# Performance work log

Measured on AMD Instinct MI355X. Metric: run time of the kernel, lower is better.

The kernel has to match this reference:

```python
import jax, jax.numpy as jnp
import numpy as np

S, B, D, H, DH = 2048, 2, 512, 8, 64
SCALE = 1.0 / DH ** 0.5
EPS = 1e-5
LN_EPS = 1e-5


def setup_inputs() -> dict:
    key = jax.random.key(0)
    k1, k2, k3, k4 = jax.random.split(key, 4)
    h = jax.random.normal(k1, (S, B, D), dtype=jnp.float32)
    # causal mask, True = masked out, shape [qlen, klen, 1] (dim==3 branch)
    attn_mask = jnp.triu(jnp.ones((S, S), dtype=bool), k=1)[:, :, None]
    Wq = jax.random.normal(k2, (D, H * DH), dtype=jnp.float32) * 0.02
    Wkv = jax.random.normal(k3, (D, 2 * H * DH), dtype=jnp.float32) * 0.02
    Wo = jax.random.normal(k4, (H * DH, D), dtype=jnp.float32) * 0.02
    gamma = jnp.ones((D,), dtype=jnp.float32)
    beta = jnp.zeros((D,), dtype=jnp.float32)
    return {"h": h, "Wq": Wq, "Wkv": Wkv, "Wo": Wo,
            "gamma": gamma, "beta": beta, "attn_mask": attn_mask}


def _layer_norm(x, gamma, beta):
    mu = jnp.mean(x, axis=-1, keepdims=True)
    var = jnp.mean(jnp.square(x - mu), axis=-1, keepdims=True)
    return (x - mu) * jax.lax.rsqrt(var + LN_EPS) * gamma + beta


def reference(h, Wq, Wkv, Wo, gamma, beta, attn_mask):
    # mems=None, pre_lnorm=False, dropout=dropatt=0 (eval)
    c = h
    head_q = (h @ Wq).reshape(S, B, H, DH)
    kv = (c @ Wkv)
    head_k, head_v = jnp.split(kv, 2, axis=-1)
    head_k = head_k.reshape(S, B, H, DH)
    head_v = head_v.reshape(S, B, H, DH)
    # elu(x) + 1 feature map
    head_q = jax.nn.elu(head_q) + 1.0
    head_k = jax.nn.elu(head_k) + 1.0
    # quadratic score matrix [i, j, b, n]
    attn_score = jnp.einsum('ibnd,jbnd->ijbn', head_q, head_k) * SCALE
    # dim==3 mask: [qlen, klen, 1] -> [qlen, klen, 1, 1], fill with 0
    attn_score = jnp.where(attn_mask[:, :, :, None], 0.0, attn_score)
    # sum-normalize over key axis (dim 1 = j)
    denominator = jnp.sum(attn_score, axis=1, keepdims=True) + EPS
    attn_prob = attn_score / denominator
    attn_vec = jnp.einsum('ijbn,jbnd->ibnd', attn_prob, head_v)
    attn_vec = attn_vec.reshape(S, B, H * DH)
    attn_out = attn_vec @ Wo
    # post-lnorm residual
    return _layer_norm(h + attn_out, gamma, beta)
```

## Files before the change

### kernel.cpp

```cpp
#include <hip/hip_runtime.h>
#include <hip/hip_bf16.h>
#include <math.h>

#define SCALE 0.125f
#define EPS 1e-5f
#define LN_EPS 1e-5f

typedef short short8 __attribute__((ext_vector_type(8)));
typedef float floatx4 __attribute__((ext_vector_type(4)));
typedef unsigned short us;

__device__ __forceinline__ float elu1(float x) { return x > 0.f ? x + 1.f : __expf(x); }
__device__ __forceinline__ us f2bf(float f) {
    __hip_bfloat16 b = __float2bfloat16(f);
    return __builtin_bit_cast(us, b);
}
__device__ __forceinline__ void gload_lds16(const void* g, void* lds) {
    __builtin_amdgcn_global_load_lds(
        (const __attribute__((address_space(1))) unsigned int*)g,
        (__attribute__((address_space(3))) unsigned int*)lds, 16, 0, 0);
}
__device__ __forceinline__ floatx4 mfma_bf16(short8 a, short8 b, floatx4 c) {
    return __builtin_amdgcn_mfma_f32_16x16x32_bf16(a, b, c, 0, 0, 0);
}

__global__ __launch_bounds__(256)
void pack_kernel(const float* __restrict__ h, const float* __restrict__ Wq,
                 const float* __restrict__ Wkv, const float* __restrict__ Wo,
                 us* __restrict__ hB, us* __restrict__ WqkvT, us* __restrict__ WoT,
                 us* __restrict__ VTg) {
    const int bid = blockIdx.x, tid = threadIdx.x;
    if (bid < 2048) {
        int idx = bid * 1024 + tid * 4;
        float4 v = *(const float4*)(h + idx);
        ushort4 o;
        o.x = f2bf(v.x); o.y = f2bf(v.y); o.z = f2bf(v.z); o.w = f2bf(v.w);
        *(ushort4*)(hB + idx) = o;
        return;
    }
    if (bid < 2304) {
        __shared__ us T[64][72];
        const float* src; int ld, n0s, k0; us* dst;
        if (bid < 2240) {
            int t2 = bid - 2048;
            int nt = t2 % 24, kt = t2 / 24;
            int n0 = nt * 64; k0 = kt * 64;
            if (n0 < 512) { src = Wq; ld = 512; n0s = n0; }
            else          { src = Wkv; ld = 1024; n0s = n0 - 512; }
            dst = WqkvT + (size_t)n0 * 512;
        } else {
            int t2 = bid - 2240;
            int nt = t2 & 7, kt = t2 >> 3;
            src = Wo; ld = 512; n0s = nt * 64; k0 = kt * 64;
            dst = WoT + (size_t)(nt * 64) * 512;
        }
        {
            int k = tid >> 2, cs = (tid & 3) * 16;
            const float* p = src + (size_t)(k0 + k) * ld + n0s + cs;
#pragma unroll
            for (int q = 0; q < 4; ++q) {
                float4 v = *(const float4*)(p + q * 4);
                T[k][cs + q * 4 + 0] = f2bf(v.x);
                T[k][cs + q * 4 + 1] = f2bf(v.y);
                T[k][cs + q * 4 + 2] = f2bf(v.z);
                T[k][cs + q * 4 + 3] = f2bf(v.w);
            }
        }
        __syncthreads();
        {
            int n = tid >> 2, ks = (tid & 3) * 16;
            __align__(16) us tmp[16];
#pragma unroll
            for (int j = 0; j < 16; ++j) tmp[j] = T[ks + j][n];
            us* po = dst + (size_t)n * 512 + k0 + ks;
            *(uint4*)(po) = *(uint4*)(tmp);
            *(uint4*)(po + 8) = *(uint4*)(tmp + 8);
        }
        return;
    }
    {
        int e = (bid - 2304) * 1024 + tid * 4;
        int chain = e >> 11, s = e & 2047;
        ushort4 o; o.x = 0x3f80; o.y = 0x3f80; o.z = 0x3f80; o.w = 0x3f80;
        *(ushort4*)(VTg + ((size_t)(chain * 80 + 64)) * 2048 + s) = o;
    }
}

__global__ __launch_bounds__(256)
void qkv_gemm(const us* __restrict__ A, const us* __restrict__ BT,
              us* __restrict__ Qg, us* __restrict__ Kg, us* __restrict__ Vg) {
    __shared__ __align__(16) us As[2][128 * 32];
    __shared__ __align__(16) us Bs[2][128 * 32];
    const int tid = threadIdx.x;
    const int w = tid >> 6, l = tid & 63;
    const int m0 = blockIdx.y * 128, n0 = blockIdx.x * 128;
    const int wm = (w >> 1) * 64, wn = (w & 1) * 64;
    floatx4 acc[4][4];
#pragma unroll
    for (int i = 0; i < 4; ++i)
#pragma unroll
        for (int j = 0; j < 4; ++j)
#pragma unroll
            for (int e = 0; e < 4; ++e) acc[i][j][e] = 0.f;

    auto STAGE = [&](int buf, int kt) {
#pragma unroll
        for (int r = 0; r < 2; ++r) {
            int slot = (r * 4 + w) * 64 + l;
            int row = slot >> 2, part = slot & 3;
            int g = part ^ (row & 3);
            gload_lds16(A + (size_t)(m0 + row) * 512 + kt + g * 8, &As[buf][(r * 4 + w) * 512]);
            gload_lds16(BT + (size_t)(n0 + row) * 512 + kt + g * 8, &Bs[buf][(r * 4 + w) * 512]);
        }
    };

    STAGE(0, 0);
    __syncthreads();
    for (int t = 0; t < 16; ++t) {
        int cur = t & 1;
        if (t < 15) STAGE(cur ^ 1, (t + 1) * 32);
        short8 a[4], b[4];
#pragma unroll
        for (int mi = 0; mi < 4; ++mi) {
            int row = wm + mi * 16 + (l & 15);
            int p = (l >> 4) ^ (row & 3);
            a[mi] = *(const short8*)(&As[cur][row * 32 + p * 8]);
        }
#pragma unroll
        for (int ni = 0; ni < 4; ++ni) {
            int row = wn + ni * 16 + (l & 15);
            int p = (l >> 4) ^ (row & 3);
            b[ni] = *(const short8*)(&Bs[cur][row * 32 + p * 8]);
        }
#pragma unroll
        for (int mi = 0; mi < 4; ++mi)
#pragma unroll
            for (int ni = 0; ni < 4; ++ni)
                acc[mi][ni] = mfma_bf16(a[mi], b[ni], acc[mi][ni]);
        __syncthreads();
    }
    const int region = blockIdx.x >> 2;
    us* outp = region == 0 ? Qg : (region == 1 ? Kg : Vg);
    const int cb = n0 - region * 512;
#pragma unroll
    for (int mi = 0; mi < 4; ++mi)
#pragma unroll
        for (int ni = 0; ni < 4; ++ni)
#pragma unroll
            for (int r = 0; r < 4; ++r) {
                int row = m0 + wm + mi * 16 + (l >> 4) * 4 + r;
                int col = cb + wn + ni * 16 + (l & 15);
                float v = acc[mi][ni][r];
                if (region < 2) v = elu1(v);
                outp[(size_t)row * 512 + col] = f2bf(v);
            }
}

__global__ __launch_bounds__(256)
void chunk_kv_kernel(const us* __restrict__ Kg, const us* __restrict__ Vg,
                     float* __restrict__ KVc, us* __restrict__ VTg) {
    __shared__ __align__(16) us VT_l[80 * 72];
    __shared__ __align__(16) us KT_l[64 * 72];
    const int c = blockIdx.x, chain = blockIdx.y;
    const int b = chain >> 3, hh = chain & 7;
    const int tid = threadIdx.x;
    const int w = tid >> 6, l = tid & 63;
#pragma unroll
    for (int gi = 0; gi < 2; ++gi) {
        int g = w + gi * 4;
        __align__(16) us vv[8];
        __align__(16) us kk[8];
#pragma unroll
        for (int e = 0; e < 8; ++e) {
            size_t off = (size_t)((c * 64 + g * 8 + e) * 2 + b) * 512 + hh * 64 + l;
            vv[e] = Vg[off];
            kk[e] = Kg[off];
        }
        *(uint4*)(VT_l + l * 72 + g * 8) = *(uint4*)vv;
        *(uint4*)(KT_l + l * 72 + g * 8) = *(uint4*)kk;
        *(uint4*)(VTg + ((size_t)(chain * 80 + l)) * 2048 + c * 64 + g * 8) = *(uint4*)vv;
    }
    if (tid < 8) {
        ushort4 o; o.x = 0x3f80; o.y = 0x3f80; o.z = 0x3f80; o.w = 0x3f80;
        *(ushort4*)(VT_l + 64 * 72 + tid * 8) = o;
        *(ushort4*)(VT_l + 64 * 72 + tid * 8 + 4) = o;
    }
    __syncthreads();
    const int l15 = l & 15, l4 = l >> 4;
    short8 af[5][2], bfr[2];
#pragma unroll
    for (int mi = 0; mi < 5; ++mi) {
        int row = mi * 16 + l15;
        af[mi][0] = *(const short8*)(VT_l + row * 72 + l4 * 8);
        af[mi][1] = *(const short8*)(VT_l + row * 72 + 32 + l4 * 8);
    }
    {
        int row = w * 16 + l15;
        bfr[0] = *(const short8*)(KT_l + row * 72 + l4 * 8);
        bfr[1] = *(const short8*)(KT_l + row * 72 + 32 + l4 * 8);
    }
    float* out = KVc + (size_t)(chain * 32 + c) * 4608;
#pragma unroll
    for (int mi = 0; mi < 5; ++mi) {
        floatx4 a = {0.f, 0.f, 0.f, 0.f};
        a = mfma_bf16(af[mi][0], bfr[0], a);
        a = mfma_bf16(af[mi][1], bfr[1], a);
#pragma unroll
        for (int r = 0; r < 4; ++r) {
            int row = mi * 16 + l4 * 4 + r;
            if (row < 65) out[row * 64 + w * 16 + l15] = a[r];
        }
    }
}

__global__ __launch_bounds__(256)
void cumsum_kernel(const float* __restrict__ KVc, us* __restrict__ MTg) {
    const int chain = blockIdx.x, rg = blockIdx.y;
    const int row = rg * 4 + (threadIdx.x >> 6), col = threadIdx.x & 63;
    const float* in = KVc + (size_t)chain * 32 * 4608 + row * 64 + col;
    us* out = MTg + ((size_t)chain * 32 * 80 + row) * 64 + col;
    float acc = 0.f;
#pragma unroll 4
    for (int cc = 0; cc < 32; ++cc) {
        out[(size_t)cc * 5120] = f2bf(acc);
        acc += in[(size_t)cc * 4608];
    }
}

__global__ __launch_bounds__(256)
void attn_kernel(const us* __restrict__ Qg, const us* __restrict__ Kg,
                 const us* __restrict__ VTg, const us* __restrict__ MTg,
                 us* __restrict__ ATT) {
    __shared__ __align__(16) us Qs[64 * 64];
    __shared__ __align__(16) us Ks[64 * 64];
    __shared__ __align__(16) us Vs[80 * 64];
    __shared__ __align__(16) us Ms[80 * 64];
    __shared__ __align__(16) us Sl[64 * 64];
    const int c = blockIdx.x, chain = blockIdx.y;
    const int b = chain >> 3, hh = chain & 7;
    const int tid = threadIdx.x;
    const int w = tid >> 6, l = tid & 63;
    const int l15 = l & 15, l4 = l >> 4;
    const int lrow = l >> 3, lg = l & 7;

#pragma unroll
    for (int r = 0; r < 2; ++r) {
        int slot = r * 4 + w;
        int row = slot * 8 + lrow;
        int g = lg ^ (row & 7);
        size_t grow = (size_t)((c * 64 + row) * 2 + b) * 512 + hh * 64 + g * 8;
        gload_lds16(Qg + grow, Qs + slot * 512);
        gload_lds16(Kg + grow, Ks + slot * 512);
    }
#pragma unroll
    for (int r = 0; r < 3; ++r) {
        int slot = r * 4 + w;
        if (slot < 10) {
            int row = slot * 8 + lrow;
            int g = lg ^ (row & 7);
            gload_lds16(VTg + (size_t)(chain * 80 + row) * 2048 + c * 64 + g * 8,
                        Vs + slot * 512);
            gload_lds16(MTg + ((size_t)(chain * 32 + c) * 80 + row) * 64 + g * 8,
                        Ms + slot * 512);
        }
    }
    __syncthreads();

    short8 qf[2];
    {
        int row = w * 16 + l15, p = l4 ^ (row & 7);
        qf[0] = *(const short8*)(Qs + row * 64 + p * 8);
        qf[1] = *(const short8*)(Qs + row * 64 + (p ^ 4) * 8);
    }
    short8 kf[4][2];
#pragma unroll
    for (int ni = 0; ni < 4; ++ni) {
        int row = ni * 16 + l15, p = l4 ^ (row & 7);
        kf[ni][0] = *(const short8*)(Ks + row * 64 + p * 8);
        kf[ni][1] = *(const short8*)(Ks + row * 64 + (p ^ 4) * 8);
    }
    short8 vf[5][2], mf[5][2];
#pragma unroll
    for (int ni = 0; ni < 5; ++ni) {
        int row = ni * 16 + l15, p = l4 ^ (row & 7);
        vf[ni][0] = *(const short8*)(Vs + row * 64 + p * 8);
        vf[ni][1] = *(const short8*)(Vs + row * 64 + (p ^ 4) * 8);
        mf[ni][0] = *(const short8*)(Ms + row * 64 + p * 8);
        mf[ni][1] = *(const short8*)(Ms + row * 64 + (p ^ 4) * 8);
    }

    const int ibase = w * 16 + l4 * 4;
#pragma unroll
    for (int ni = 0; ni < 4; ++ni) {
        floatx4 s = {0.f, 0.f, 0.f, 0.f};
        s = mfma_bf16(qf[0], kf[ni][0], s);
        s = mfma_bf16(qf[1], kf[ni][1], s);
        int col = ni * 16 + l15;
#pragma unroll
        for (int r = 0; r < 4; ++r) {
            int i = ibase + r;
            float v = (col <= i) ? s[r] : 0.f;
            Sl[i * 64 + (((col >> 3) ^ (i & 7)) * 8) + (col & 7)] = f2bf(v);
        }
    }
    __syncthreads();

    short8 sf[2];
    {
        int ir = w * 16 + l15;
        sf[0] = *(const short8*)(Sl + ir * 64 + ((l4 ^ (ir & 7)) * 8));
        sf[1] = *(const short8*)(Sl + ir * 64 + (((4 + l4) ^ (ir & 7)) * 8));
    }

    floatx4 acc[5];
#pragma unroll
    for (int ni = 0; ni < 5; ++ni) {
        floatx4 a = {0.f, 0.f, 0.f, 0.f};
        a = mfma_bf16(sf[0], vf[ni][0], a);
        a = mfma_bf16(sf[1], vf[ni][1], a);
        a = mfma_bf16(qf[0], mf[ni][0], a);
        a = mfma_bf16(qf[1], mf[ni][1], a);
        acc[ni] = a;
    }

    float fac[4];
#pragma unroll
    for (int r = 0; r < 4; ++r) {
        float den = __shfl(acc[4][r], l & 48, 64);
        fac[r] = SCALE / (SCALE * den + EPS);
    }
#pragma unroll
    for (int ni = 0; ni < 4; ++ni)
#pragma unroll
        for (int r = 0; r < 4; ++r) {
            int i = ibase + r;
            ATT[((size_t)((c * 64 + i) * 2 + b)) * 512 + hh * 64 + ni * 16 + l15] =
                f2bf(acc[ni][r] * fac[r]);
        }
}

__global__ __launch_bounds__(256)
void wo_ln_kernel(const us* __restrict__ ATT, const us* __restrict__ WoT,
                  const float* __restrict__ h, const float* __restrict__ gamma,
                  const float* __restrict__ beta, float* __restrict__ out) {
    __shared__ __align__(16) us As[2][16 * 32];
    __shared__ __align__(16) us Bs[2][512 * 32];
    __shared__ float redS[4][16];
    __shared__ float redQ[4][16];
    __shared__ float mml[16], rsl[16];
    const int tid = threadIdx.x;
    const int w = tid >> 6, l = tid & 63;
    const int l15 = l & 15, l4 = l >> 4;
    const int m0 = blockIdx.x * 16, wn = w * 128;
    floatx4 acc[8];
#pragma unroll
    for (int j = 0; j < 8; ++j)
#pragma unroll
        for (int e = 0; e < 4; ++e) acc[j][e] = 0.f;

    auto STAGE = [&](int buf, int kt) {
#pragma unroll
        for (int r = 0; r < 8; ++r) {
            int slot = r * 4 + w;
            int row = slot * 16 + (l >> 2);
            int g = (l & 3) ^ (row & 3);
            gload_lds16(WoT + (size_t)row * 512 + kt + g * 8, &Bs[buf][slot * 512]);
        }
        if (w == 0) {
            int row = l >> 2;
            int g = (l & 3) ^ (row & 3);
            gload_lds16(ATT + (size_t)(m0 + row) * 512 + kt + g * 8, &As[buf][0]);
        }
    };

    STAGE(0, 0);
    __syncthreads();
    for (int t = 0; t < 16; ++t) {
        int cur = t & 1;
        if (t < 15) STAGE(cur ^ 1, (t + 1) * 32);
        short8 af, bf[8];
        {
            int row = l15, p = l4 ^ (row & 3);
            af = *(const short8*)(&As[cur][row * 32 + p * 8]);
        }
#pragma unroll
        for (int ni = 0; ni < 8; ++ni) {
            int row = wn + ni * 16 + l15, p = l4 ^ (row & 3);
            bf[ni] = *(const short8*)(&Bs[cur][row * 32 + p * 8]);
        }
#pragma unroll
        for (int ni = 0; ni < 8; ++ni)
            acc[ni] = mfma_bf16(af, bf[ni], acc[ni]);
        __syncthreads();
    }

#pragma unroll
    for (int r = 0; r < 4; ++r) {
        int row = l4 * 4 + r;
        const float* hrow = h + (size_t)(m0 + row) * 512 + wn + l15;
        float s = 0.f, q = 0.f;
#pragma unroll
        for (int ni = 0; ni < 8; ++ni) {
            float x = acc[ni][r] + hrow[ni * 16];
            acc[ni][r] = x;
            s += x;
            q = fmaf(x, x, q);
        }
#pragma unroll
        for (int off = 1; off <= 8; off <<= 1) {
            s += __shfl_xor(s, off, 64);
            q += __shfl_xor(q, off, 64);
        }
        if (l15 == 0) { redS[w][row] = s; redQ[w][row] = q; }
    }
    __syncthreads();
    if (tid < 16) {
        float s = redS[0][tid] + redS[1][tid] + redS[2][tid] + redS[3][tid];
        float q = redQ[0][tid] + redQ[1][tid] + redQ[2][tid] + redQ[3][tid];
        float mean = s * (1.f / 512);
        float var = q * (1.f / 512) - mean * mean;
        mml[tid] = mean;
        rsl[tid] = rsqrtf(var + LN_EPS);
    }
    __syncthreads();
#pragma unroll
    for (int r = 0; r < 4; ++r) {
        int row = l4 * 4 + r;
        float mean = mml[row], rstd = rsl[row];
#pragma unroll
        for (int ni = 0; ni < 8; ++ni) {
            int col = wn + ni * 16 + l15;
            out[(size_t)(m0 + row) * 512 + col] =
                (acc[ni][r] - mean) * rstd * gamma[col] + beta[col];
        }
    }
}

extern "C" void kernel_launch(void* const* d_in, const int* in_sizes, int n_in,
                              void* d_out, int out_size, void* d_ws, size_t ws_size,
                              hipStream_t stream) {
    const float* h = (const float*)d_in[0];
    const float* Wq = (const float*)d_in[1];
    const float* Wkv = (const float*)d_in[2];
    const float* Wo = (const float*)d_in[3];
    const float* gamma = (const float*)d_in[4];
    const float* beta = (const float*)d_in[5];

    char* ws = (char*)d_ws;
    us* Qg      = (us*)(ws + 0);
    us* Kg      = (us*)(ws + 4194304);
    us* Vg      = (us*)(ws + 8388608);
    us* VTg     = (us*)(ws + 12582912);
    us* ATT     = (us*)(ws + 17825792);
    us* WoT     = (us*)(ws + 22020096);
    us* MTg     = (us*)(ws + 22544384);
    us* hB      = (us*)(ws + 27787264);
    us* WqkvT   = (us*)(ws + 31981568);
    float* KVc  = (float*)(ws + 33554432);

    dim3 blk(256);
    pack_kernel<<<2336, blk, 0, stream>>>(h, Wq, Wkv, Wo, hB, WqkvT, WoT, VTg);
    qkv_gemm<<<dim3(12, 32), blk, 0, stream>>>(hB, WqkvT, Qg, Kg, Vg);
    chunk_kv_kernel<<<dim3(32, 16), blk, 0, stream>>>(Kg, Vg, KVc, VTg);
    cumsum_kernel<<<dim3(16, 17), blk, 0, stream>>>(KVc, MTg);
    attn_kernel<<<dim3(32, 16), blk, 0, stream>>>(Qg, Kg, VTg, MTg, ATT);
    wo_ln_kernel<<<256, blk, 0, stream>>>(ATT, WoT, h, gamma, beta, (float*)d_out);
}
```

Measured before the change: 134.7 us.

## Write V transposed from QKV GEMM epilogue and overlap attn loads with QK compute

The QKV GEMM's M tile is halved to 64 rows, doubling the grid. Its V region now writes directly into the transposed VTg layout, so the separate V buffer is gone and chunk_kv no longer gathers and transposes V. chunk_kv instead loads the V^T tile with async LDS loads and a swizzled layout. In attn_kernel, a partial vmcnt wait lets the QK^T score computation start while the V and M tiles are still loading. The transposed epilogue does strided 4-byte stores, and the smaller GEMM tile gives less reuse per block.

```diff
diff --git a/kernel.cpp b/kernel.cpp
--- a/kernel.cpp
+++ b/kernel.cpp
@@ -88,29 +88,35 @@
 
 __global__ __launch_bounds__(256)
 void qkv_gemm(const us* __restrict__ A, const us* __restrict__ BT,
-              us* __restrict__ Qg, us* __restrict__ Kg, us* __restrict__ Vg) {
-    __shared__ __align__(16) us As[2][128 * 32];
+              us* __restrict__ Qg, us* __restrict__ Kg, us* __restrict__ VTg) {
+    __shared__ __align__(16) us As[2][64 * 32];
     __shared__ __align__(16) us Bs[2][128 * 32];
     const int tid = threadIdx.x;
     const int w = tid >> 6, l = tid & 63;
-    const int m0 = blockIdx.y * 128, n0 = blockIdx.x * 128;
-    const int wm = (w >> 1) * 64, wn = (w & 1) * 64;
-    floatx4 acc[4][4];
-#pragma unroll
-    for (int i = 0; i < 4; ++i)
+    const int l15 = l & 15, l4 = l >> 4;
+    const int bx = blockIdx.x;
+    const int m0 = blockIdx.y * 64, n0 = bx * 128;
+    const int wm = (w >> 1) * 32, wn = (w & 1) * 64;
+    floatx4 acc[2][4];
+#pragma unroll
+    for (int i = 0; i < 2; ++i)
 #pragma unroll
         for (int j = 0; j < 4; ++j)
 #pragma unroll
             for (int e = 0; e < 4; ++e) acc[i][j][e] = 0.f;
 
     auto STAGE = [&](int buf, int kt) {
+        {
+            int row = w * 16 + (l >> 2);
+            int g = (l & 3) ^ (row & 3);
+            gload_lds16(A + (size_t)(m0 + row) * 512 + kt + g * 8, &As[buf][w * 512]);
+        }
 #pragma unroll
         for (int r = 0; r < 2; ++r) {
-            int slot = (r * 4 + w) * 64 + l;
-            int row = slot >> 2, part = slot & 3;
-            int g = part ^ (row & 3);
-            gload_lds16(A + (size_t)(m0 + row) * 512 + kt + g * 8, &As[buf][(r * 4 + w) * 512]);
-            gload_lds16(BT + (size_t)(n0 + row) * 512 + kt + g * 8, &Bs[buf][(r * 4 + w) * 512]);
+            int slot = r * 4 + w;
+            int row = slot * 16 + (l >> 2);
+            int g = (l & 3) ^ (row & 3);
+            gload_lds16(BT + (size_t)(n0 + row) * 512 + kt + g * 8, &Bs[buf][slot * 512]);
         }
     };
 
@@ -119,71 +125,88 @@
     for (int t = 0; t < 16; ++t) {
         int cur = t & 1;
         if (t < 15) STAGE(cur ^ 1, (t + 1) * 32);
-        short8 a[4], b[4];
-#pragma unroll
-        for (int mi = 0; mi < 4; ++mi) {
-            int row = wm + mi * 16 + (l & 15);
-            int p = (l >> 4) ^ (row & 3);
+        short8 a[2], b[4];
+#pragma unroll
+        for (int mi = 0; mi < 2; ++mi) {
+            int row = wm + mi * 16 + l15;
+            int p = l4 ^ (row & 3);
             a[mi] = *(const short8*)(&As[cur][row * 32 + p * 8]);
         }
 #pragma unroll
         for (int ni = 0; ni < 4; ++ni) {
-            int row = wn + ni * 16 + (l & 15);
-            int p = (l >> 4) ^ (row & 3);
+            int row = wn + ni * 16 + l15;
+            int p = l4 ^ (row & 3);
             b[ni] = *(const short8*)(&Bs[cur][row * 32 + p * 8]);
         }
 #pragma unroll
-        for (int mi = 0; mi < 4; ++mi)
+        for (int mi = 0; mi < 2; ++mi)
 #pragma unroll
             for (int ni = 0; ni < 4; ++ni)
                 acc[mi][ni] = mfma_bf16(a[mi], b[ni], acc[mi][ni]);
         __syncthreads();
     }
-    const int region = blockIdx.x >> 2;
-    us* outp = region == 0 ? Qg : (region == 1 ? Kg : Vg);
-    const int cb = n0 - region * 512;
-#pragma unroll
-    for (int mi = 0; mi < 4; ++mi)
-#pragma unroll
-        for (int ni = 0; ni < 4; ++ni)
-#pragma unroll
-            for (int r = 0; r < 4; ++r) {
-                int row = m0 + wm + mi * 16 + (l >> 4) * 4 + r;
-                int col = cb + wn + ni * 16 + (l & 15);
-                float v = acc[mi][ni][r];
-                if (region < 2) v = elu1(v);
-                outp[(size_t)row * 512 + col] = f2bf(v);
+    const int region = bx >> 2;
+    const int cb = (bx & 3) * 128;
+    if (region < 2) {
+        us* outp = region == 0 ? Qg : Kg;
+#pragma unroll
+        for (int mi = 0; mi < 2; ++mi)
+#pragma unroll
+            for (int ni = 0; ni < 4; ++ni)
+#pragma unroll
+                for (int r = 0; r < 4; ++r) {
+                    int row = m0 + wm + mi * 16 + l4 * 4 + r;
+                    int col = cb + wn + ni * 16 + l15;
+                    outp[(size_t)row * 512 + col] = f2bf(elu1(acc[mi][ni][r]));
+                }
+    } else {
+        const int hh = (bx & 3) * 2 + (w & 1);
+#pragma unroll
+        for (int mi = 0; mi < 2; ++mi) {
+            int row0 = m0 + wm + mi * 16 + l4 * 4;
+            int s0 = row0 >> 1;
+#pragma unroll
+            for (int ni = 0; ni < 4; ++ni) {
+                int d = ni * 16 + l15;
+#pragma unroll
+                for (int b = 0; b < 2; ++b) {
+                    unsigned int pk = (unsigned int)f2bf(acc[mi][ni][b]) |
+                                      ((unsigned int)f2bf(acc[mi][ni][2 + b]) << 16);
+                    *(unsigned int*)(VTg + ((size_t)((b * 8 + hh) * 80 + d)) * 2048 + s0) = pk;
+                }
             }
-}
-
-__global__ __launch_bounds__(256)
-void chunk_kv_kernel(const us* __restrict__ Kg, const us* __restrict__ Vg,
-                     float* __restrict__ KVc, us* __restrict__ VTg) {
-    __shared__ __align__(16) us VT_l[80 * 72];
+        }
+    }
+}
+
+__global__ __launch_bounds__(256)
+void chunk_kv_kernel(const us* __restrict__ Kg, const us* __restrict__ VTg,
+                     float* __restrict__ KVc) {
+    __shared__ __align__(16) us VT_l[80 * 64];
     __shared__ __align__(16) us KT_l[64 * 72];
     const int c = blockIdx.x, chain = blockIdx.y;
     const int b = chain >> 3, hh = chain & 7;
     const int tid = threadIdx.x;
     const int w = tid >> 6, l = tid & 63;
+    const int lrow = l >> 3, lg = l & 7;
+#pragma unroll
+    for (int r = 0; r < 3; ++r) {
+        int slot = r * 4 + w;
+        if (slot < 10) {
+            int row = slot * 8 + lrow;
+            int g = lg ^ (row & 7);
+            gload_lds16(VTg + (size_t)(chain * 80 + row) * 2048 + c * 64 + g * 8,
+                        VT_l + slot * 512);
+        }
+    }
 #pragma unroll
     for (int gi = 0; gi < 2; ++gi) {
         int g = w + gi * 4;
-        __align__(16) us vv[8];
         __align__(16) us kk[8];
 #pragma unroll
-        for (int e = 0; e < 8; ++e) {
-            size_t off = (size_t)((c * 64 + g * 8 + e) * 2 + b) * 512 + hh * 64 + l;
-            vv[e] = Vg[off];
-            kk[e] = Kg[off];
-        }
-        *(uint4*)(VT_l + l * 72 + g * 8) = *(uint4*)vv;
+        for (int e = 0; e < 8; ++e)
+            kk[e] = Kg[(size_t)((c * 64 + g * 8 + e) * 2 + b) * 512 + hh * 64 + l];
         *(uint4*)(KT_l + l * 72 + g * 8) = *(uint4*)kk;
-        *(uint4*)(VTg + ((size_t)(chain * 80 + l)) * 2048 + c * 64 + g * 8) = *(uint4*)vv;
-    }
-    if (tid < 8) {
-        ushort4 o; o.x = 0x3f80; o.y = 0x3f80; o.z = 0x3f80; o.w = 0x3f80;
-        *(ushort4*)(VT_l + 64 * 72 + tid * 8) = o;
-        *(ushort4*)(VT_l + 64 * 72 + tid * 8 + 4) = o;
     }
     __syncthreads();
     const int l15 = l & 15, l4 = l >> 4;
@@ -191,8 +214,9 @@
 #pragma unroll
     for (int mi = 0; mi < 5; ++mi) {
         int row = mi * 16 + l15;
-        af[mi][0] = *(const short8*)(VT_l + row * 72 + l4 * 8);
-        af[mi][1] = *(const short8*)(VT_l + row * 72 + 32 + l4 * 8);
+        int p = l4 ^ (row & 7);
+        af[mi][0] = *(const short8*)(VT_l + row * 64 + p * 8);
+        af[mi][1] = *(const short8*)(VT_l + row * 64 + (p ^ 4) * 8);
     }
     {
         int row = w * 16 + l15;
@@ -253,18 +277,21 @@
         gload_lds16(Kg + grow, Ks + slot * 512);
     }
 #pragma unroll
-    for (int r = 0; r < 3; ++r) {
-        int slot = r * 4 + w;
-        if (slot < 10) {
-            int row = slot * 8 + lrow;
-            int g = lg ^ (row & 7);
+    for (int i = 0; i < 5; ++i) {
+        int p = w * 5 + i;
+        int s = p < 10 ? p : p - 10;
+        int row = s * 8 + lrow;
+        int g = lg ^ (row & 7);
+        if (p < 10)
             gload_lds16(VTg + (size_t)(chain * 80 + row) * 2048 + c * 64 + g * 8,
-                        Vs + slot * 512);
+                        Vs + s * 512);
+        else
             gload_lds16(MTg + ((size_t)(chain * 32 + c) * 80 + row) * 64 + g * 8,
-                        Ms + slot * 512);
-        }
-    }
-    __syncthreads();
+                        Ms + s * 512);
+    }
+    asm volatile("s_waitcnt vmcnt(5)" ::: "memory");
+    __builtin_amdgcn_sched_barrier(0);
+    __builtin_amdgcn_s_barrier();
 
     short8 qf[2];
     {
@@ -279,6 +306,29 @@
         kf[ni][0] = *(const short8*)(Ks + row * 64 + p * 8);
         kf[ni][1] = *(const short8*)(Ks + row * 64 + (p ^ 4) * 8);
     }
+
+    const int ibase = w * 16 + l4 * 4;
+#pragma unroll
+    for (int ni = 0; ni < 4; ++ni) {
+        floatx4 s = {0.f, 0.f, 0.f, 0.f};
+        s = mfma_bf16(qf[0], kf[ni][0], s);
+        s = mfma_bf16(qf[1], kf[ni][1], s);
+        int col = ni * 16 + l15;
+#pragma unroll
+        for (int r = 0; r < 4; ++r) {
+            int i = ibase + r;
+            float v = (col <= i) ? s[r] : 0.f;
+            Sl[i * 64 + (((col >> 3) ^ (i & 7)) * 8) + (col & 7)] = f2bf(v);
+        }
+    }
+    short8 sf[2];
+    {
+        int ir = w * 16 + l15;
+        sf[0] = *(const short8*)(Sl + ir * 64 + ((l4 ^ (ir & 7)) * 8));
+        sf[1] = *(const short8*)(Sl + ir * 64 + (((4 + l4) ^ (ir & 7)) * 8));
+    }
+    __syncthreads();
+
     short8 vf[5][2], mf[5][2];
 #pragma unroll
     for (int ni = 0; ni < 5; ++ni) {
@@ -287,29 +337,6 @@
         vf[ni][1] = *(const short8*)(Vs + row * 64 + (p ^ 4) * 8);
         mf[ni][0] = *(const short8*)(Ms + row * 64 + p * 8);
         mf[ni][1] = *(const short8*)(Ms + row * 64 + (p ^ 4) * 8);
-    }
-
-    const int ibase = w * 16 + l4 * 4;
-#pragma unroll
-    for (int ni = 0; ni < 4; ++ni) {
-        floatx4 s = {0.f, 0.f, 0.f, 0.f};
-        s = mfma_bf16(qf[0], kf[ni][0], s);
-        s = mfma_bf16(qf[1], kf[ni][1], s);
-        int col = ni * 16 + l15;
-#pragma unroll
-        for (int r = 0; r < 4; ++r) {
-            int i = ibase + r;
-            float v = (col <= i) ? s[r] : 0.f;
-            Sl[i * 64 + (((col >> 3) ^ (i & 7)) * 8) + (col & 7)] = f2bf(v);
-        }
-    }
-    __syncthreads();
-
-    short8 sf[2];
-    {
-        int ir = w * 16 + l15;
-        sf[0] = *(const short8*)(Sl + ir * 64 + ((l4 ^ (ir & 7)) * 8));
-        sf[1] = *(const short8*)(Sl + ir * 64 + (((4 + l4) ^ (ir & 7)) * 8));
     }
 
     floatx4 acc[5];
@@ -449,7 +476,6 @@
     char* ws = (char*)d_ws;
     us* Qg      = (us*)(ws + 0);
     us* Kg      = (us*)(ws + 4194304);
-    us* Vg      = (us*)(ws + 8388608);
     us* VTg     = (us*)(ws + 12582912);
     us* ATT     = (us*)(ws + 17825792);
     us* WoT     = (us*)(ws + 22020096);
@@ -460,8 +486,8 @@
 
     dim3 blk(256);
     pack_kernel<<<2336, blk, 0, stream>>>(h, Wq, Wkv, Wo, hB, WqkvT, WoT, VTg);
-    qkv_gemm<<<dim3(12, 32), blk, 0, stream>>>(hB, WqkvT, Qg, Kg, Vg);
-    chunk_kv_kernel<<<dim3(32, 16), blk, 0, stream>>>(Kg, Vg, KVc, VTg);
+    qkv_gemm<<<dim3(12, 64), blk, 0, stream>>>(hB, WqkvT, Qg, Kg, VTg);
+    chunk_kv_kernel<<<dim3(32, 16), blk, 0, stream>>>(Kg, VTg, KVc);
     cumsum_kernel<<<dim3(16, 17), blk, 0, stream>>>(KVc, MTg);
     attn_kernel<<<dim3(32, 16), blk, 0, stream>>>(Qg, Kg, VTg, MTg, ATT);
     wo_ln_kernel<<<256, blk, 0, stream>>>(ATT, WoT, h, gamma, beta, (float*)d_out);
```

New measurement: 132.7 us. No clear change (-1.4%).
